# Performance work log

Hardware: AMD Instinct MI355X
Metric: run time of the kernel (lower is better)

The kernel has to match this reference:

```python
import jax, jax.numpy as jnp
import numpy as np

TEMP = 0.07      # InfoNCE temperature
NB = 15          # neighborhood side length
HALF = NB // 2
NUM_SAMPLES = 256
EPS = 1e-8       # F.cosine_similarity eps


def setup_inputs() -> dict:
    key = jax.random.key(0)
    k1, k2, k3, k4 = jax.random.split(key, 4)
    B, D, H, W = 8, 128, 256, 256
    features = jax.random.normal(k1, (B, D, H, W), jnp.float32)
    targets = jax.random.randint(k2, (B, H, W), 0, 4, jnp.int32)
    # anchors restricted to the valid interior [HALF, H-HALF)
    anchor_h = jax.random.randint(k3, (B, NUM_SAMPLES), HALF, H - HALF, jnp.int32)
    anchor_w = jax.random.randint(k4, (B, NUM_SAMPLES), HALF, W - HALF, jnp.int32)
    return {"features": features, "targets": targets,
            "anchor_h": anchor_h, "anchor_w": anchor_w}


def _local_contrastive_loss(features, targets, anchor_h, anchor_w):
    offs = jnp.arange(-HALF, HALF + 1)  # (NB,)

    def per_image(feat, lab, ah, aw):
        # feat: (D,H,W), lab: (H,W), ah/aw: (N,)
        N = ah.shape[0]
        wh = jnp.broadcast_to(ah[:, None, None] + offs[None, :, None], (N, NB, NB))
        ww = jnp.broadcast_to(aw[:, None, None] + offs[None, None, :], (N, NB, NB))
        patch = feat[:, wh, ww]          # (D, N, NB, NB) gathered local windows
        plab = lab[wh, ww]               # (N, NB, NB)
        af = feat[:, ah, aw]             # (D, N) anchor features
        alab = lab[ah, aw]               # (N,)
        # cosine similarity (with eps clamp like F.cosine_similarity), / temperature
        an = jnp.maximum(jnp.sqrt(jnp.sum(af * af, axis=0)), EPS)          # (N,)
        pn = jnp.maximum(jnp.sqrt(jnp.sum(patch * patch, axis=0)), EPS)    # (N,NB,NB)
        sim = jnp.einsum('dn,dnkl->nkl', af, patch) / (an[:, None, None] * pn) / TEMP
        # positive mask: same label, centre pixel excluded
        pos = plab == alab[:, None, None]
        pos = pos.at[:, HALF, HALF].set(False)
        sim_flat = sim.reshape(N, -1)                 # (N, NB*NB)
        pos_flat = pos.reshape(N, -1)
        pos_cnt = pos_flat.sum(-1)                    # (N,)
        lse = jax.nn.logsumexp(sim_flat, axis=-1)     # (N,)
        pos_mean = jnp.where(pos_flat, sim_flat, 0.0).sum(-1) / jnp.maximum(pos_cnt, 1)
        valid = pos_cnt > 0
        loss_i = -(pos_mean - lse)
        return jnp.where(valid, loss_i, 0.0).sum(), valid.sum()

    losses, counts = jax.vmap(per_image)(features, targets, anchor_h, anchor_w)
    total = losses.sum()
    cnt = counts.sum()
    return jnp.where(cnt > 0,
                     total / jnp.maximum(cnt, 1).astype(total.dtype),
                     jnp.zeros((), total.dtype))


def reference(features, targets, anchor_h, anchor_w):
    return _local_contrastive_loss(features, targets, anchor_h, anchor_w)
```

## Files before the change

### kernel.cpp

```cpp
#include <hip/hip_runtime.h>
#include <math.h>

#define TEMPC   0.07f
#define NBK     15
#define HALFK   7
#define NPOS    225
#define DD      128
#define HHH     256
#define WWW     256
#define PLANE   (HHH * WWW)
#define NSAMP   256
#define EPSC    1e-8f

#define CCH     32
#define NCH     (DD / CCH)
#define GRP     16
#define MAXA    256
#define MAXP    (MAXA * NBK)

__global__ __launch_bounds__(256) void k_afgather(
    const float* __restrict__ feat,
    const int*   __restrict__ anch_h,
    const int*   __restrict__ anch_w,
    float*       __restrict__ afg,
    int n_anchors)
{
    int idx = blockIdx.x * 256 + threadIdx.x;
    if (idx >= n_anchors * DD) return;
    int bn = idx >> 7;
    int d  = idx & 127;
    int b  = bn >> 8;
    int ah = anch_h[bn], aw = anch_w[bn];
    afg[idx] = feat[(size_t)b * DD * PLANE + d * PLANE + ah * WWW + aw];
}

__global__ __launch_bounds__(256) void k_sweep(
    const float* __restrict__ feat,
    const int*   __restrict__ anch_h,
    const int*   __restrict__ anch_w,
    const float* __restrict__ afg,
    float*       __restrict__ dot_out,
    float*       __restrict__ normimg)
{
    const int bh   = blockIdx.x;
    const int b    = bh >> 8;
    const int h    = bh & 255;
    const int tid  = threadIdx.x;
    const int lane = tid & 63;
    const int wave = tid >> 6;

    __shared__ float rows[CCH][WWW];
    __shared__ float dacc[MAXP];
    __shared__ float afl[GRP][33];
    __shared__ int   s_n[MAXA], s_aw[MAXA], s_k[MAXA];
    __shared__ int   wcnt[4];

    const int ah_t = anch_h[b * NSAMP + tid];
    const bool in  = (ah_t - h <= HALFK) && (h - ah_t <= HALFK);
    unsigned long long m = __ballot(in);
    if (lane == 0) wcnt[wave] = __popcll(m);
    __syncthreads();
    const int ncnt = wcnt[0] + wcnt[1] + wcnt[2] + wcnt[3];
    if (in) {
        int base = 0;
        #pragma unroll
        for (int w = 0; w < 4; ++w) if (w < wave) base += wcnt[w];
        int p = base + __popcll(m & ((1ULL << lane) - 1ULL));
        s_n[p]  = tid;
        s_aw[p] = anch_w[b * NSAMP + tid];
        s_k[p]  = h - ah_t + HALFK;
    }
    __syncthreads();
    if (ncnt == 0) return;

    const int npos = ncnt * NBK;
    for (int p = tid; p < npos; p += 256) dacc[p] = 0.f;

    const float* fbh = feat + (size_t)b * DD * PLANE + h * WWW;
    const int ngrp = (ncnt + GRP - 1) / GRP;
    float nrm = 0.f;

    for (int c = 0; c < NCH; ++c) {
        const int ch0 = c * CCH;
        __syncthreads();
        #pragma unroll
        for (int i = 0; i < 8; ++i) {
            int f  = i * 256 + tid;
            int ch = f >> 6;
            int c4 = f & 63;
            *(float4*)&rows[ch][c4 * 4] =
                *(const float4*)&fbh[(size_t)(ch0 + ch) * PLANE + c4 * 4];
        }
        __syncthreads();
        #pragma unroll
        for (int ch = 0; ch < CCH; ++ch) {
            float v = rows[ch][tid];
            nrm = fmaf(v, v, nrm);
        }
        for (int g = 0; g < ngrp; ++g) {
            const int a0 = g * GRP;
            const int na = min(GRP, ncnt - a0);
            __syncthreads();
            for (int f = tid; f < na * CCH; f += 256) {
                int j = f >> 5, cc = f & 31;
                afl[j][cc] = afg[(size_t)(b * NSAMP + s_n[a0 + j]) * DD + ch0 + cc];
            }
            __syncthreads();
            const int np = na * NBK;
            if (tid < np) {
                int j    = tid / NBK;
                int cpos = tid - j * NBK;
                int col  = s_aw[a0 + j] - HALFK + cpos;
                float dsum = 0.f;
                #pragma unroll
                for (int ch = 0; ch < CCH; ++ch)
                    dsum = fmaf(afl[j][ch], rows[ch][col], dsum);
                dacc[a0 * NBK + tid] += dsum;
            }
        }
    }

    normimg[(b * HHH + h) * WWW + tid] = nrm;
    __syncthreads();
    for (int p = tid; p < npos; p += 256) {
        int slot = p / NBK;
        int cpos = p - slot * NBK;
        int bn   = b * NSAMP + s_n[slot];
        dot_out[bn * NPOS + s_k[slot] * NBK + cpos] = dacc[p];
    }
}

__global__ __launch_bounds__(256) void k_softmax(
    const int*   __restrict__ targ,
    const int*   __restrict__ anch_h,
    const int*   __restrict__ anch_w,
    const float* __restrict__ dot_out,
    const float* __restrict__ normimg,
    float*       __restrict__ loss_part,
    float*       __restrict__ cnt_part)
{
    const int bn   = blockIdx.x;
    const int b    = bn >> 8;
    const int tid  = threadIdx.x;
    const int lane = tid & 63;
    const int wave = tid >> 6;
    __shared__ float red[4], red2[4], red3[4];
    __shared__ float s_max;

    const int ah = anch_h[bn], aw = anch_w[bn];
    const int* lab = targ + b * PLANE;
    const int alab = lab[ah * WWW + aw];
    const float an = fmaxf(sqrtf(normimg[(b * HHH + ah) * WWW + aw]), EPSC);

    const bool active = tid < NPOS;
    float sim = -INFINITY;
    bool  pos = false;
    if (active) {
        int k  = tid / NBK, l = tid - (tid / NBK) * NBK;
        int hh = ah - HALFK + k, ww = aw - HALFK + l;
        float dot = dot_out[bn * NPOS + tid];
        float pn  = fmaxf(sqrtf(normimg[(b * HHH + hh) * WWW + ww]), EPSC);
        sim = dot / (an * pn * TEMPC);
        pos = (lab[hh * WWW + ww] == alab) && (tid != (HALFK * NBK + HALFK));
    }

    float mx = sim;
    #pragma unroll
    for (int off = 32; off; off >>= 1) mx = fmaxf(mx, __shfl_down(mx, off, 64));
    if (lane == 0) red[wave] = mx;
    __syncthreads();
    if (tid == 0) s_max = fmaxf(fmaxf(red[0], red[1]), fmaxf(red[2], red[3]));
    __syncthreads();
    mx = s_max;

    float e  = active ? expf(sim - mx) : 0.f;
    float ps = pos ? sim : 0.f;
    float pc = pos ? 1.f : 0.f;
    #pragma unroll
    for (int off = 32; off; off >>= 1) {
        e  += __shfl_down(e,  off, 64);
        ps += __shfl_down(ps, off, 64);
        pc += __shfl_down(pc, off, 64);
    }
    if (lane == 0) { red[wave] = e; red2[wave] = ps; red3[wave] = pc; }
    __syncthreads();
    if (tid == 0) {
        float E  = red[0]  + red[1]  + red[2]  + red[3];
        float PS = red2[0] + red2[1] + red2[2] + red2[3];
        float PC = red3[0] + red3[1] + red3[2] + red3[3];
        float lse = mx + logf(E);
        bool valid = PC > 0.5f;
        loss_part[bn] = valid ? (lse - PS / PC) : 0.f;
        cnt_part[bn]  = valid ? 1.f : 0.f;
    }
}

__global__ __launch_bounds__(256) void lcl_finalize(
    const float* __restrict__ loss_part,
    const float* __restrict__ cnt_part,
    float*       __restrict__ out,
    int n)
{
    const int tid  = threadIdx.x;
    const int lane = tid & 63;
    const int wave = tid >> 6;
    __shared__ float rs[4], rc[4];

    float s = 0.f, c = 0.f;
    for (int i = tid; i < n; i += 256) {
        s += loss_part[i];
        c += cnt_part[i];
    }
    #pragma unroll
    for (int off = 32; off; off >>= 1) {
        s += __shfl_down(s, off, 64);
        c += __shfl_down(c, off, 64);
    }
    if (lane == 0) { rs[wave] = s; rc[wave] = c; }
    __syncthreads();
    if (tid == 0) {
        float S = rs[0] + rs[1] + rs[2] + rs[3];
        float C = rc[0] + rc[1] + rc[2] + rc[3];
        out[0] = (C > 0.5f) ? (S / C) : 0.f;
    }
}

extern "C" void kernel_launch(void* const* d_in, const int* in_sizes, int n_in,
                              void* d_out, int out_size, void* d_ws, size_t ws_size,
                              hipStream_t stream) {
    const float* feat  = (const float*)d_in[0];
    const int*   targ  = (const int*)d_in[1];
    const int*   anchh = (const int*)d_in[2];
    const int*   anchw = (const int*)d_in[3];
    float* out = (float*)d_out;

    const int n_anchors = in_sizes[2];
    const int B = n_anchors / NSAMP;

    float* afg       = (float*)d_ws;
    float* dot_out   = afg      + (size_t)n_anchors * DD;
    float* normimg   = dot_out  + (size_t)n_anchors * NPOS;
    float* loss_part = normimg  + (size_t)B * PLANE;
    float* cnt_part  = loss_part + n_anchors;

    k_afgather<<<(n_anchors * DD + 255) / 256, 256, 0, stream>>>(
        feat, anchh, anchw, afg, n_anchors);
    k_sweep<<<B * HHH, 256, 0, stream>>>(
        feat, anchh, anchw, afg, dot_out, normimg);
    k_softmax<<<n_anchors, 256, 0, stream>>>(
        targ, anchh, anchw, dot_out, normimg, loss_part, cnt_part);
    lcl_finalize<<<1, 256, 0, stream>>>(loss_part, cnt_part, out, n_anchors);
}
```

Baseline: 378.1 us.

## Fuse norm and label work into sweep, shrink shared memory, widen anchor groups

The gather kernel now also computes each anchor's norm and label. The sweep kernel normalises dot products by the patch-pixel norm and writes the positive mask, so the softmax kernel no longer reads the full-image norm buffer or the label map. Shared dot accumulators are capped at 128 anchors per pass, with an outer loop over passes, to cut LDS use and allow 3 blocks per CU. Anchor groups double to 32 and the first group's load is merged with the row load barrier. The cost is an extra byte-mask buffer and repeated row loads when more than 128 anchors touch a row.

```diff
diff --git a/kernel.cpp b/kernel.cpp
--- a/kernel.cpp
+++ b/kernel.cpp
@@ -14,33 +14,48 @@
 
 #define CCH     32
 #define NCH     (DD / CCH)
-#define GRP     16
+#define GRP     32
+#define CAPA    128
 #define MAXA    256
-#define MAXP    (MAXA * NBK)
-
-__global__ __launch_bounds__(256) void k_afgather(
+
+__global__ __launch_bounds__(128) void k_prep(
     const float* __restrict__ feat,
+    const int*   __restrict__ targ,
     const int*   __restrict__ anch_h,
     const int*   __restrict__ anch_w,
     float*       __restrict__ afg,
-    int n_anchors)
-{
-    int idx = blockIdx.x * 256 + threadIdx.x;
-    if (idx >= n_anchors * DD) return;
-    int bn = idx >> 7;
-    int d  = idx & 127;
-    int b  = bn >> 8;
-    int ah = anch_h[bn], aw = anch_w[bn];
-    afg[idx] = feat[(size_t)b * DD * PLANE + d * PLANE + ah * WWW + aw];
-}
-
-__global__ __launch_bounds__(256) void k_sweep(
+    float*       __restrict__ anorm,
+    int*         __restrict__ alab_g)
+{
+    const int bn = blockIdx.x;
+    const int b  = bn >> 8;
+    const int d  = threadIdx.x;
+    const int ah = anch_h[bn], aw = anch_w[bn];
+
+    float v = feat[(size_t)b * DD * PLANE + (size_t)d * PLANE + ah * WWW + aw];
+    afg[(size_t)bn * DD + d] = v;
+
+    float s = v * v;
+    #pragma unroll
+    for (int off = 32; off; off >>= 1) s += __shfl_down(s, off, 64);
+    __shared__ float r2[2];
+    if ((d & 63) == 0) r2[d >> 6] = s;
+    __syncthreads();
+    if (d == 0) {
+        anorm[bn]  = fmaxf(sqrtf(r2[0] + r2[1]), EPSC);
+        alab_g[bn] = targ[b * PLANE + ah * WWW + aw];
+    }
+}
+
+__global__ __launch_bounds__(256, 3) void k_sweep(
     const float* __restrict__ feat,
     const int*   __restrict__ anch_h,
     const int*   __restrict__ anch_w,
     const float* __restrict__ afg,
-    float*       __restrict__ dot_out,
-    float*       __restrict__ normimg)
+    const int*   __restrict__ alab_g,
+    const int*   __restrict__ targ,
+    float*       __restrict__ simn,
+    unsigned char* __restrict__ posm)
 {
     const int bh   = blockIdx.x;
     const int b    = bh >> 8;
@@ -49,119 +64,130 @@
     const int lane = tid & 63;
     const int wave = tid >> 6;
 
-    __shared__ float rows[CCH][WWW];
-    __shared__ float dacc[MAXP];
-    __shared__ float afl[GRP][33];
-    __shared__ int   s_n[MAXA], s_aw[MAXA], s_k[MAXA];
+    __shared__ __align__(16) float rows[CCH][WWW];
+    __shared__ float dacc[CAPA * NBK];
+    __shared__ float afl[GRP][CCH + 1];
+    __shared__ float pn_s[WWW];
+    __shared__ int   labs[WWW];
+    __shared__ int   s_n[MAXA], s_aw[MAXA], s_alab[MAXA], s_k[MAXA];
     __shared__ int   wcnt[4];
 
     const int ah_t = anch_h[b * NSAMP + tid];
     const bool in  = (ah_t - h <= HALFK) && (h - ah_t <= HALFK);
     unsigned long long m = __ballot(in);
     if (lane == 0) wcnt[wave] = __popcll(m);
+    labs[tid] = targ[b * PLANE + h * WWW + tid];
     __syncthreads();
     const int ncnt = wcnt[0] + wcnt[1] + wcnt[2] + wcnt[3];
     if (in) {
-        int base = 0;
+        int base0 = 0;
         #pragma unroll
-        for (int w = 0; w < 4; ++w) if (w < wave) base += wcnt[w];
-        int p = base + __popcll(m & ((1ULL << lane) - 1ULL));
-        s_n[p]  = tid;
-        s_aw[p] = anch_w[b * NSAMP + tid];
-        s_k[p]  = h - ah_t + HALFK;
+        for (int w = 0; w < 4; ++w) if (w < wave) base0 += wcnt[w];
+        int p = base0 + __popcll(m & ((1ULL << lane) - 1ULL));
+        s_n[p]    = tid;
+        s_aw[p]   = anch_w[b * NSAMP + tid];
+        s_alab[p] = alab_g[b * NSAMP + tid];
+        s_k[p]    = h - ah_t + HALFK;
     }
     __syncthreads();
     if (ncnt == 0) return;
 
-    const int npos = ncnt * NBK;
-    for (int p = tid; p < npos; p += 256) dacc[p] = 0.f;
-
     const float* fbh = feat + (size_t)b * DD * PLANE + h * WWW;
-    const int ngrp = (ncnt + GRP - 1) / GRP;
     float nrm = 0.f;
 
-    for (int c = 0; c < NCH; ++c) {
-        const int ch0 = c * CCH;
+    for (int base = 0; base < ncnt; base += CAPA) {
+        const int nloc  = min(CAPA, ncnt - base);
+        const int nposl = nloc * NBK;
+        const int ngrp  = (nloc + GRP - 1) / GRP;
+        for (int p = tid; p < nposl; p += 256) dacc[p] = 0.f;
+
+        for (int c = 0; c < NCH; ++c) {
+            const int ch0 = c * CCH;
+            __syncthreads();
+            #pragma unroll
+            for (int i = 0; i < 8; ++i) {
+                int f  = i * 256 + tid;
+                int ch = f >> 6;
+                int c4 = f & 63;
+                *(float4*)&rows[ch][c4 * 4] =
+                    *(const float4*)&fbh[(size_t)(ch0 + ch) * PLANE + c4 * 4];
+            }
+            {
+                const int na = min(GRP, nloc);
+                for (int f = tid; f < na * CCH; f += 256) {
+                    int j = f >> 5, cc = f & 31;
+                    afl[j][cc] = afg[(size_t)(b * NSAMP + s_n[base + j]) * DD + ch0 + cc];
+                }
+            }
+            __syncthreads();
+            if (base == 0) {
+                #pragma unroll
+                for (int ch = 0; ch < CCH; ++ch) {
+                    float v = rows[ch][tid];
+                    nrm = fmaf(v, v, nrm);
+                }
+            }
+            for (int g = 0; g < ngrp; ++g) {
+                const int a0 = g * GRP;
+                const int na = min(GRP, nloc - a0);
+                if (g > 0) {
+                    __syncthreads();
+                    for (int f = tid; f < na * CCH; f += 256) {
+                        int j = f >> 5, cc = f & 31;
+                        afl[j][cc] = afg[(size_t)(b * NSAMP + s_n[base + a0 + j]) * DD + ch0 + cc];
+                    }
+                    __syncthreads();
+                }
+                for (int p = tid; p < na * NBK; p += 256) {
+                    int j    = p / NBK;
+                    int cpos = p - j * NBK;
+                    int col  = s_aw[base + a0 + j] - HALFK + cpos;
+                    float dsum = 0.f;
+                    #pragma unroll
+                    for (int ch = 0; ch < CCH; ++ch)
+                        dsum = fmaf(afl[j][ch], rows[ch][col], dsum);
+                    dacc[(a0 + j) * NBK + cpos] += dsum;
+                }
+            }
+        }
+        if (base == 0) pn_s[tid] = fmaxf(sqrtf(nrm), EPSC);
         __syncthreads();
-        #pragma unroll
-        for (int i = 0; i < 8; ++i) {
-            int f  = i * 256 + tid;
-            int ch = f >> 6;
-            int c4 = f & 63;
-            *(float4*)&rows[ch][c4 * 4] =
-                *(const float4*)&fbh[(size_t)(ch0 + ch) * PLANE + c4 * 4];
+
+        for (int p = tid; p < nposl; p += 256) {
+            int slot = p / NBK;
+            int cpos = p - slot * NBK;
+            int a    = base + slot;
+            int bn   = b * NSAMP + s_n[a];
+            int col  = s_aw[a] - HALFK + cpos;
+            int o    = bn * NPOS + s_k[a] * NBK + cpos;
+            simn[o] = dacc[p] / pn_s[col];
+            posm[o] = (labs[col] == s_alab[a]) ? 1 : 0;
         }
         __syncthreads();
-        #pragma unroll
-        for (int ch = 0; ch < CCH; ++ch) {
-            float v = rows[ch][tid];
-            nrm = fmaf(v, v, nrm);
-        }
-        for (int g = 0; g < ngrp; ++g) {
-            const int a0 = g * GRP;
-            const int na = min(GRP, ncnt - a0);
-            __syncthreads();
-            for (int f = tid; f < na * CCH; f += 256) {
-                int j = f >> 5, cc = f & 31;
-                afl[j][cc] = afg[(size_t)(b * NSAMP + s_n[a0 + j]) * DD + ch0 + cc];
-            }
-            __syncthreads();
-            const int np = na * NBK;
-            if (tid < np) {
-                int j    = tid / NBK;
-                int cpos = tid - j * NBK;
-                int col  = s_aw[a0 + j] - HALFK + cpos;
-                float dsum = 0.f;
-                #pragma unroll
-                for (int ch = 0; ch < CCH; ++ch)
-                    dsum = fmaf(afl[j][ch], rows[ch][col], dsum);
-                dacc[a0 * NBK + tid] += dsum;
-            }
-        }
-    }
-
-    normimg[(b * HHH + h) * WWW + tid] = nrm;
-    __syncthreads();
-    for (int p = tid; p < npos; p += 256) {
-        int slot = p / NBK;
-        int cpos = p - slot * NBK;
-        int bn   = b * NSAMP + s_n[slot];
-        dot_out[bn * NPOS + s_k[slot] * NBK + cpos] = dacc[p];
     }
 }
 
 __global__ __launch_bounds__(256) void k_softmax(
-    const int*   __restrict__ targ,
-    const int*   __restrict__ anch_h,
-    const int*   __restrict__ anch_w,
-    const float* __restrict__ dot_out,
-    const float* __restrict__ normimg,
-    float*       __restrict__ loss_part,
-    float*       __restrict__ cnt_part)
+    const float*         __restrict__ simn,
+    const unsigned char* __restrict__ posm,
+    const float*         __restrict__ anorm,
+    float*               __restrict__ loss_part,
+    float*               __restrict__ cnt_part)
 {
     const int bn   = blockIdx.x;
-    const int b    = bn >> 8;
     const int tid  = threadIdx.x;
     const int lane = tid & 63;
     const int wave = tid >> 6;
     __shared__ float red[4], red2[4], red3[4];
     __shared__ float s_max;
 
-    const int ah = anch_h[bn], aw = anch_w[bn];
-    const int* lab = targ + b * PLANE;
-    const int alab = lab[ah * WWW + aw];
-    const float an = fmaxf(sqrtf(normimg[(b * HHH + ah) * WWW + aw]), EPSC);
-
     const bool active = tid < NPOS;
     float sim = -INFINITY;
     bool  pos = false;
     if (active) {
-        int k  = tid / NBK, l = tid - (tid / NBK) * NBK;
-        int hh = ah - HALFK + k, ww = aw - HALFK + l;
-        float dot = dot_out[bn * NPOS + tid];
-        float pn  = fmaxf(sqrtf(normimg[(b * HHH + hh) * WWW + ww]), EPSC);
-        sim = dot / (an * pn * TEMPC);
-        pos = (lab[hh * WWW + ww] == alab) && (tid != (HALFK * NBK + HALFK));
+        float sc = 1.0f / (anorm[bn] * TEMPC);
+        sim = simn[bn * NPOS + tid] * sc;
+        pos = posm[bn * NPOS + tid] && (tid != (HALFK * NBK + HALFK));
     }
 
     float mx = sim;
@@ -238,16 +264,18 @@
     const int B = n_anchors / NSAMP;
 
     float* afg       = (float*)d_ws;
-    float* dot_out   = afg      + (size_t)n_anchors * DD;
-    float* normimg   = dot_out  + (size_t)n_anchors * NPOS;
-    float* loss_part = normimg  + (size_t)B * PLANE;
+    float* anorm     = afg       + (size_t)n_anchors * DD;
+    float* simn      = anorm     + n_anchors;
+    float* loss_part = simn      + (size_t)n_anchors * NPOS;
     float* cnt_part  = loss_part + n_anchors;
-
-    k_afgather<<<(n_anchors * DD + 255) / 256, 256, 0, stream>>>(
-        feat, anchh, anchw, afg, n_anchors);
-    k_sweep<<<B * HHH, 256, 0, stream>>>(
-        feat, anchh, anchw, afg, dot_out, normimg);
-    k_softmax<<<n_anchors, 256, 0, stream>>>(
-        targ, anchh, anchw, dot_out, normimg, loss_part, cnt_part);
+    int*   alab_g    = (int*)(cnt_part + n_anchors);
+    unsigned char* posm = (unsigned char*)(alab_g + n_anchors);
+
+    k_prep<<<n_anchors, 128, 0, stream>>>(feat, targ, anchh, anchw,
+                                          afg, anorm, alab_g);
+    k_sweep<<<B * HHH, 256, 0, stream>>>(feat, anchh, anchw, afg, alab_g, targ,
+                                         simn, posm);
+    k_softmax<<<n_anchors, 256, 0, stream>>>(simn, posm, anorm,
+                                             loss_part, cnt_part);
     lcl_finalize<<<1, 256, 0, stream>>>(loss_part, cnt_part, out, n_anchors);
 }
```

After: 383.3 us. About the same (+1.4%).
